# Kernel optimization log

Measured on AMD Instinct MI355X. Metric: run time of the kernel, lower is better.

Reference implementation:

```python
import jax, jax.numpy as jnp
import numpy as np

N, E, M = 50000, 50000, 640000
IN_DIM, D, L = 256, 128, 3

def setup_inputs() -> dict:
    key = jax.random.key(0)
    ks = jax.random.split(key, 8)
    x = jax.random.normal(ks[0], (N, IN_DIM), dtype=jnp.float32)
    hyperedge_index = jax.random.randint(ks[1], (2, M), 0, N, dtype=jnp.int64)
    weightMatrix = jax.random.uniform(ks[2], (E,), dtype=jnp.float32)
    edgesWeights = jax.random.uniform(ks[3], (M,), dtype=jnp.float32)
    stdv_fc = 1.0 / np.sqrt(IN_DIM)
    fc_w = jax.random.uniform(ks[4], (IN_DIM, D), minval=-stdv_fc, maxval=stdv_fc, dtype=jnp.float32)
    fc_b = jax.random.uniform(ks[5], (D,), minval=-stdv_fc, maxval=stdv_fc, dtype=jnp.float32)
    stdv = 1.0 / np.sqrt(D)
    conv_w = jax.random.uniform(ks[6], (L, D, D), minval=-stdv, maxval=stdv, dtype=jnp.float32)
    conv_b = jax.random.uniform(ks[7], (L, D), minval=-stdv, maxval=stdv, dtype=jnp.float32)
    return {"x": x, "hyperedge_index": hyperedge_index, "weightMatrix": weightMatrix,
            "edgesWeights": edgesWeights, "fc_w": fc_w, "fc_b": fc_b,
            "conv_w": conv_w, "conv_b": conv_b}

def reference(x, hyperedge_index, weightMatrix, edgesWeights, fc_w, fc_b, conv_w, conv_b):
    row, col = hyperedge_index[0], hyperedge_index[1]
    n_nodes, n_edges = x.shape[0], weightMatrix.shape[0]
    # degree normalization (computed once, shared by all layers since inputs identical)
    node_deg = jax.ops.segment_sum(weightMatrix[col], row, num_segments=n_nodes) + 1e-8
    hyper_deg = jax.ops.segment_sum(edgesWeights, col, num_segments=n_edges) + 1e-8
    nd = node_deg ** -0.5
    nd = jnp.where(jnp.isinf(nd), 0.0, nd)
    hd = hyper_deg ** -0.5
    hd = jnp.where(jnp.isinf(hd), 0.0, hd)
    norm = hd[col] * nd[row]  # [M]
    h = jax.nn.relu(x @ fc_w + fc_b)  # [N, D]; dropout inactive (eval)
    for i in range(conv_w.shape[0]):
        xt = h @ conv_w[i] + conv_b[i]                                  # [N, D]
        wx = xt[row] * (edgesWeights * norm)[:, None]                   # [M, D]
        hyper_feat = jax.ops.segment_sum(wx, col, num_segments=n_edges)  # [E, D]
        wh = hyper_feat[col] * (weightMatrix[col] * edgesWeights * norm)[:, None]  # [M, D]
        z = jax.ops.segment_sum(wh, row, num_segments=n_nodes)           # [N, D]
        h = jax.nn.relu(h + z)
    return h
```

## Files before the change

kernel.cpp:

```cpp
#include <hip/hip_runtime.h>
#include <hip/hip_bf16.h>
#include <stdint.h>

typedef __attribute__((ext_vector_type(4))) float f4;
typedef __attribute__((ext_vector_type(2))) float f2;
typedef __attribute__((ext_vector_type(2))) int i2;
typedef __attribute__((ext_vector_type(8))) unsigned short us8;
typedef __attribute__((ext_vector_type(4))) unsigned short us4;
typedef __attribute__((ext_vector_type(2))) unsigned short us2;
typedef __attribute__((ext_vector_type(8))) short s8b;
typedef __attribute__((ext_vector_type(4))) float f32x4;

#define CW_SHIFT 7
#define CH 2048

__device__ __forceinline__ float bf2f(unsigned short u) {
  union { unsigned int i; float f; } t; t.i = ((unsigned int)u) << 16; return t.f;
}
__device__ __forceinline__ unsigned short f2bf(float f) {
  union { float f; unsigned int i; } t; t.f = f;
  unsigned int u = t.i;
  return (unsigned short)((u + 0x7FFFu + ((u >> 16) & 1u)) >> 16);
}
__device__ __forceinline__ float cvtload(const void* p, int i, int f16) {
  return f16 ? bf2f(((const unsigned short*)p)[i]) : ((const float*)p)[i];
}

__global__ void detect_kernel(const unsigned int* __restrict__ xb,
                              const unsigned int* __restrict__ ib,
                              int* __restrict__ flags) {
  if (threadIdx.x == 0) {
    int cnt = 0;
    for (int i = 0; i < 256; ++i) {
      unsigned int e = (xb[i] >> 7) & 0xffu;
      if (e >= 110u && e <= 135u) ++cnt;
    }
    flags[0] = (cnt >= 180) ? 1 : 0;
    int zc = 0;
    for (int i = 0; i < 128; ++i) if (ib[2 * i + 1] == 0u) ++zc;
    flags[1] = (zc >= 120) ? 1 : 0;
  }
}

__global__ void cvt_params(const void* __restrict__ wM, const void* __restrict__ fcw,
                           const void* __restrict__ fcb, const void* __restrict__ cw,
                           const void* __restrict__ cb,
                           float* __restrict__ WMf, unsigned short* __restrict__ FCWT,
                           float* __restrict__ FCB, unsigned short* __restrict__ CWT,
                           float* __restrict__ CBf,
                           int E, int L, const int* __restrict__ flags) {
  const int IN_DIM = 256, D = 128;
  int i = blockIdx.x * 256 + threadIdx.x;
  const int f16 = flags[0];
  if (i < E) { WMf[i] = cvtload(wM, i, f16); return; }
  i -= E;
  if (i < IN_DIM * D) {
    int c = i >> 8, k = i & 255;
    FCWT[i] = f2bf(cvtload(fcw, k * D + c, f16));
    return;
  }
  i -= IN_DIM * D;
  if (i < D) { FCB[i] = cvtload(fcb, i, f16); return; }
  i -= D;
  if (i < L * D * D) {
    int l = i >> 14, rem = i & 16383;
    int c = rem >> 7, k = rem & 127;
    CWT[i] = f2bf(cvtload(cw, l * D * D + k * D + c, f16));
    return;
  }
  i -= L * D * D;
  if (i < L * D) CBf[i] = cvtload(cb, i, f16);
}

__global__ __launch_bounds__(256) void bin_count(
    const void* __restrict__ hei, int M, int* __restrict__ cntAB,
    int nbE, int nbN, int nblk, const int* __restrict__ flags) {
  __shared__ int hA[512];
  __shared__ int hB[512];
  const int tid = threadIdx.x, blk = blockIdx.x;
  for (int b = tid; b < 512; b += 256) { hA[b] = 0; hB[b] = 0; }
  __syncthreads();
  const int i64 = flags[1];
#pragma unroll
  for (int i = 0; i < CH / 256; ++i) {
    int m = blk * CH + i * 256 + tid;
    if (m >= M) break;
    int r, c;
    if (i64) {
      r = (int)((const long long*)hei)[m];
      c = (int)((const long long*)hei)[M + m];
    } else {
      r = ((const int*)hei)[m];
      c = ((const int*)hei)[M + m];
    }
    atomicAdd(&hA[c >> CW_SHIFT], 1);
    atomicAdd(&hB[r >> CW_SHIFT], 1);
  }
  __syncthreads();
  for (int b = tid; b < nbE; b += 256) cntAB[b * nblk + blk] = hA[b];
  for (int b = tid; b < nbN; b += 256) cntAB[(nbE + b) * nblk + blk] = hB[b];
}

__global__ __launch_bounds__(512) void scanA(int* __restrict__ cnt,
                                             int* __restrict__ btot, int nblk) {
  __shared__ int sc[512];
  const int tid = threadIdx.x, b = blockIdx.x;
  int v = (tid < nblk) ? cnt[b * nblk + tid] : 0;
  sc[tid] = v;
  __syncthreads();
  for (int s = 1; s < 512; s <<= 1) {
    int t = (tid >= s) ? sc[tid - s] : 0;
    __syncthreads();
    sc[tid] += t;
    __syncthreads();
  }
  if (tid < nblk) cnt[b * nblk + tid] = sc[tid] - v;
  if (tid == 511) btot[b] = sc[511];
}

__global__ __launch_bounds__(512) void scanB(const int* __restrict__ btot,
                                             int* __restrict__ bbaseA,
                                             int* __restrict__ bbaseB,
                                             int nbE, int nbN) {
  __shared__ int sc[512];
  const int tid = threadIdx.x;
  const int nb = blockIdx.x ? nbN : nbE;
  const int* src = blockIdx.x ? (btot + nbE) : btot;
  int* dst = blockIdx.x ? bbaseB : bbaseA;
  int v = (tid < nb) ? src[tid] : 0;
  sc[tid] = v;
  __syncthreads();
  for (int s = 1; s < 512; s <<= 1) {
    int t = (tid >= s) ? sc[tid - s] : 0;
    __syncthreads();
    sc[tid] += t;
    __syncthreads();
  }
  if (tid < nb) dst[tid] = sc[tid] - v;
  if (tid == 511) dst[nb] = sc[511];
}

__global__ __launch_bounds__(256) void binscatter(
    const void* __restrict__ hei, const void* __restrict__ ew, int M,
    const int* __restrict__ cntAB,
    const int* __restrict__ bbaseA, const int* __restrict__ bbaseB,
    int* __restrict__ KEYA, i2* __restrict__ PAYA,
    int* __restrict__ KEYB, i2* __restrict__ PAYB,
    int nbE, int nbN, int nblk, const int* __restrict__ flags) {
  __shared__ int baseA[512];
  __shared__ int baseB[512];
  const int tid = threadIdx.x, blk = blockIdx.x;
  for (int b = tid; b < nbE; b += 256) baseA[b] = bbaseA[b] + cntAB[b * nblk + blk];
  for (int b = tid; b < nbN; b += 256) baseB[b] = bbaseB[b] + cntAB[(nbE + b) * nblk + blk];
  __syncthreads();
  const int i64 = flags[1], f16 = flags[0];
#pragma unroll
  for (int i = 0; i < CH / 256; ++i) {
    int m = blk * CH + i * 256 + tid;
    if (m >= M) break;
    int r, c;
    if (i64) {
      r = (int)((const long long*)hei)[m];
      c = (int)((const long long*)hei)[M + m];
    } else {
      r = ((const int*)hei)[m];
      c = ((const int*)hei)[M + m];
    }
    int e = __float_as_int(f16 ? bf2f(((const unsigned short*)ew)[m])
                               : ((const float*)ew)[m]);
    int pA = atomicAdd(&baseA[c >> CW_SHIFT], 1);
    KEYA[pA] = c;
    i2 ea; ea[0] = r; ea[1] = e; PAYA[pA] = ea;
    int pB = atomicAdd(&baseB[r >> CW_SHIFT], 1);
    KEYB[pB] = r;
    i2 eb; eb[0] = c; eb[1] = e; PAYB[pB] = eb;
  }
}

__global__ __launch_bounds__(256) void finalize3(
    const int* __restrict__ KEYA, const i2* __restrict__ PAYA,
    const int* __restrict__ bbaseA, i2* __restrict__ ENTA,
    int* __restrict__ offE, int E,
    const int* __restrict__ KEYB, const i2* __restrict__ PAYB,
    const int* __restrict__ bbaseB, i2* __restrict__ ENTB,
    int* __restrict__ offN, int Nn,
    const float* __restrict__ WMf, float* __restrict__ SCE,
    float* __restrict__ ND, int nbE) {
  __shared__ int cnt[128];
  __shared__ int sc[128];
  __shared__ int cur[128];
  __shared__ float fsum[128];
  int b = blockIdx.x;
  const int* KEY; const i2* PAY; const int* bbase; i2* ENT; int* off;
  int nseg, modeB; float* outScale;
  if (b < nbE) {
    KEY = KEYA; PAY = PAYA; bbase = bbaseA; ENT = ENTA; off = offE;
    nseg = E; modeB = 0; outScale = SCE;
  } else {
    b -= nbE;
    KEY = KEYB; PAY = PAYB; bbase = bbaseB; ENT = ENTB; off = offN;
    nseg = Nn; modeB = 1; outScale = ND;
  }
  const int tid = threadIdx.x;
  const int bs = bbase[b], be = bbase[b + 1];
  const int cb = b << CW_SHIFT;
  const int cw = min(128, nseg - cb);
  if (tid < 128) { cnt[tid] = 0; fsum[tid] = 0.f; }
  __syncthreads();
  for (int k = bs + tid; k < be; k += 256) atomicAdd(&cnt[KEY[k] - cb], 1);
  __syncthreads();
  if (tid < 128) sc[tid] = cnt[tid];
  __syncthreads();
  for (int s = 1; s < 128; s <<= 1) {
    int t = (tid < 128 && tid >= s) ? sc[tid - s] : 0;
    __syncthreads();
    if (tid < 128) sc[tid] += t;
    __syncthreads();
  }
  if (tid < 128) {
    int start = bs + sc[tid] - cnt[tid];
    cur[tid] = start;
    if (tid < cw) off[cb + tid] = start;
  }
  if (tid == 0 && b == ((nseg + 127) >> CW_SHIFT) - 1) off[nseg] = be;
  __syncthreads();
  for (int k = bs + tid; k < be; k += 256) {
    int c = KEY[k] - cb;
    i2 p = PAY[k];
    int pos = atomicAdd(&cur[c], 1);
    ENT[pos] = p;
    float add = modeB ? WMf[p[0]] : __int_as_float(p[1]);
    atomicAdd(&fsum[c], add);
  }
  __syncthreads();
  if (tid < cw) {
    float s = fsum[tid] + 1e-8f;
    outScale[cb + tid] = modeB ? rsqrtf(s) : (WMf[cb + tid] / s);
  }
}

template<int KS>
__global__ __launch_bounds__(256) void gemm_mfma3(
    const void* __restrict__ Aptr, const unsigned short* __restrict__ Wt,
    const float* __restrict__ bias, unsigned short* __restrict__ out,
    int Nrows, const int* __restrict__ flags, int relu,
    const float* __restrict__ rowScale) {
  constexpr int K = KS * 32;
  constexpr int KC = K / 8;
  extern __shared__ unsigned short Bs[];
  const int tid = threadIdx.x;
  const int wv = tid >> 6, ln = tid & 63;
  const int lr = ln & 15;
  const int lk = (ln >> 4) << 3;
  const int rowBase = blockIdx.x * 128 + wv * 32;
  const int aF32 = flags ? (flags[0] ? 0 : 1) : 0;

  int ar[2];
#pragma unroll
  for (int t = 0; t < 2; ++t) {
    int r = rowBase + t * 16 + lr;
    ar[t] = (r < Nrows) ? r : (Nrows - 1);
  }

  s8b aR[2][KS];
  if (!aF32) {
#pragma unroll
    for (int t = 0; t < 2; ++t)
#pragma unroll
      for (int ks = 0; ks < KS; ++ks)
        aR[t][ks] = *reinterpret_cast<const s8b*>(
            (const unsigned short*)Aptr + (size_t)ar[t] * K + ks * 32 + lk);
  } else {
#pragma unroll
    for (int t = 0; t < 2; ++t)
#pragma unroll
      for (int ks = 0; ks < KS; ++ks) {
        const float* ap = (const float*)Aptr + (size_t)ar[t] * K + ks * 32 + lk;
        f4 u0 = *reinterpret_cast<const f4*>(ap);
        f4 u1 = *reinterpret_cast<const f4*>(ap + 4);
#pragma unroll
        for (int j = 0; j < 4; ++j) {
          aR[t][ks][j]     = (short)f2bf(u0[j]);
          aR[t][ks][4 + j] = (short)f2bf(u1[j]);
        }
      }
  }

#pragma unroll
  for (int it = 0; it < (128 * KC + 255) / 256; ++it) {
    int ch = it * 256 + tid;
    if (ch < 128 * KC) {
      int row = ch / KC, kc = (ch % KC) << 3;
      us8 v = *reinterpret_cast<const us8*>(Wt + (size_t)row * K + kc);
      int byte = ((row * K + kc) << 1) ^ ((row & 7) << 4);
      *reinterpret_cast<us8*>((char*)Bs + byte) = v;
    }
  }
  __syncthreads();

  f32x4 acc[2][8];
#pragma unroll
  for (int t = 0; t < 2; ++t)
#pragma unroll
    for (int n = 0; n < 8; ++n) acc[t][n] = (f32x4)0.f;

#pragma unroll
  for (int ks = 0; ks < KS; ++ks) {
#pragma unroll
    for (int n = 0; n < 8; ++n) {
      const int brow = n * 16 + lr;
      int byte = ((brow * K + ks * 32 + lk) << 1) ^ ((brow & 7) << 4);
      s8b b = *reinterpret_cast<const s8b*>((const char*)Bs + byte);
      acc[0][n] = __builtin_amdgcn_mfma_f32_16x16x32_bf16(aR[0][ks], b, acc[0][n], 0, 0, 0);
      acc[1][n] = __builtin_amdgcn_mfma_f32_16x16x32_bf16(aR[1][ks], b, acc[1][n], 0, 0, 0);
    }
  }

#pragma unroll
  for (int t = 0; t < 2; ++t) {
    const int orow0 = rowBase + t * 16 + ((ln >> 4) << 2);
#pragma unroll
    for (int n = 0; n < 8; ++n) {
      const int col = n * 16 + lr;
      const float bv = bias[col];
#pragma unroll
      for (int r = 0; r < 4; ++r) {
        int row = orow0 + r;
        if (row >= Nrows) continue;
        float s = acc[t][n][r] + bv;
        if (relu) s = fmaxf(s, 0.f);
        if (rowScale) s *= rowScale[row];
        out[(size_t)row * 128 + col] = f2bf(s);
      }
    }
  }
}

__global__ __launch_bounds__(256) void gather_edge3(
    const int* __restrict__ off, const i2* __restrict__ ENT,
    const float* __restrict__ sc_e, const unsigned short* __restrict__ X,
    unsigned short* __restrict__ out, int nseg) {
  int seg = blockIdx.x * 8 + (threadIdx.x >> 5);
  if (seg >= nseg) return;
  int d = (threadIdx.x & 31) << 2;
  int k0 = off[seg], k1 = off[seg + 1];
  float a0 = 0.f, a1 = 0.f, a2 = 0.f, a3 = 0.f;
  int k = k0;
  for (; k + 4 <= k1; k += 4) {
    i2 e0 = ENT[k], e1 = ENT[k + 1], e2 = ENT[k + 2], e3 = ENT[k + 3];
    us4 v0 = *reinterpret_cast<const us4*>(X + (size_t)e0[0] * 128 + d);
    us4 v1 = *reinterpret_cast<const us4*>(X + (size_t)e1[0] * 128 + d);
    us4 v2 = *reinterpret_cast<const us4*>(X + (size_t)e2[0] * 128 + d);
    us4 v3 = *reinterpret_cast<const us4*>(X + (size_t)e3[0] * 128 + d);
    float c0 = __int_as_float(e0[1]), c1 = __int_as_float(e1[1]);
    float c2 = __int_as_float(e2[1]), c3 = __int_as_float(e3[1]);
    a0 += c0 * bf2f(v0[0]); a1 += c0 * bf2f(v0[1]); a2 += c0 * bf2f(v0[2]); a3 += c0 * bf2f(v0[3]);
    a0 += c1 * bf2f(v1[0]); a1 += c1 * bf2f(v1[1]); a2 += c1 * bf2f(v1[2]); a3 += c1 * bf2f(v1[3]);
    a0 += c2 * bf2f(v2[0]); a1 += c2 * bf2f(v2[1]); a2 += c2 * bf2f(v2[2]); a3 += c2 * bf2f(v2[3]);
    a0 += c3 * bf2f(v3[0]); a1 += c3 * bf2f(v3[1]); a2 += c3 * bf2f(v3[2]); a3 += c3 * bf2f(v3[3]);
  }
  for (; k < k1; ++k) {
    i2 e = ENT[k];
    us4 v = *reinterpret_cast<const us4*>(X + (size_t)e[0] * 128 + d);
    float c = __int_as_float(e[1]);
    a0 += c * bf2f(v[0]); a1 += c * bf2f(v[1]); a2 += c * bf2f(v[2]); a3 += c * bf2f(v[3]);
  }
  float sc = sc_e[seg];
  us4 o;
  o[0] = f2bf(sc * a0); o[1] = f2bf(sc * a1); o[2] = f2bf(sc * a2); o[3] = f2bf(sc * a3);
  *reinterpret_cast<us4*>(out + (size_t)seg * 128 + d) = o;
}

__global__ __launch_bounds__(256) void gather_node3(
    const int* __restrict__ off, const i2* __restrict__ ENT,
    const float* __restrict__ nd, const unsigned short* __restrict__ HF,
    const unsigned short* __restrict__ H, void* __restrict__ out,
    int nseg, int outF32) {
  int seg = blockIdx.x * 8 + (threadIdx.x >> 5);
  if (seg >= nseg) return;
  int d = (threadIdx.x & 31) << 2;
  int k0 = off[seg], k1 = off[seg + 1];
  float a0 = 0.f, a1 = 0.f, a2 = 0.f, a3 = 0.f;
  int k = k0;
  for (; k + 4 <= k1; k += 4) {
    i2 e0 = ENT[k], e1 = ENT[k + 1], e2 = ENT[k + 2], e3 = ENT[k + 3];
    us4 v0 = *reinterpret_cast<const us4*>(HF + (size_t)e0[0] * 128 + d);
    us4 v1 = *reinterpret_cast<const us4*>(HF + (size_t)e1[0] * 128 + d);
    us4 v2 = *reinterpret_cast<const us4*>(HF + (size_t)e2[0] * 128 + d);
    us4 v3 = *reinterpret_cast<const us4*>(HF + (size_t)e3[0] * 128 + d);
    float c0 = __int_as_float(e0[1]), c1 = __int_as_float(e1[1]);
    float c2 = __int_as_float(e2[1]), c3 = __int_as_float(e3[1]);
    a0 += c0 * bf2f(v0[0]); a1 += c0 * bf2f(v0[1]); a2 += c0 * bf2f(v0[2]); a3 += c0 * bf2f(v0[3]);
    a0 += c1 * bf2f(v1[0]); a1 += c1 * bf2f(v1[1]); a2 += c1 * bf2f(v1[2]); a3 += c1 * bf2f(v1[3]);
    a0 += c2 * bf2f(v2[0]); a1 += c2 * bf2f(v2[1]); a2 += c2 * bf2f(v2[2]); a3 += c2 * bf2f(v2[3]);
    a0 += c3 * bf2f(v3[0]); a1 += c3 * bf2f(v3[1]); a2 += c3 * bf2f(v3[2]); a3 += c3 * bf2f(v3[3]);
  }
  for (; k < k1; ++k) {
    i2 e = ENT[k];
    us4 v = *reinterpret_cast<const us4*>(HF + (size_t)e[0] * 128 + d);
    float c = __int_as_float(e[1]);
    a0 += c * bf2f(v[0]); a1 += c * bf2f(v[1]); a2 += c * bf2f(v[2]); a3 += c * bf2f(v[3]);
  }
  float s = nd[seg];
  us4 h = *reinterpret_cast<const us4*>(H + (size_t)seg * 128 + d);
  float r0 = fmaxf(bf2f(h[0]) + s * a0, 0.f);
  float r1 = fmaxf(bf2f(h[1]) + s * a1, 0.f);
  float r2 = fmaxf(bf2f(h[2]) + s * a2, 0.f);
  float r3 = fmaxf(bf2f(h[3]) + s * a3, 0.f);
  if (outF32) {
    f4 o; o[0] = r0; o[1] = r1; o[2] = r2; o[3] = r3;
    *reinterpret_cast<f4*>((float*)out + (size_t)seg * 128 + d) = o;
  } else {
    us4 o; o[0] = f2bf(r0); o[1] = f2bf(r1); o[2] = f2bf(r2); o[3] = f2bf(r3);
    *reinterpret_cast<us4*>((unsigned short*)out + (size_t)seg * 128 + d) = o;
  }
}

extern "C" void kernel_launch(void* const* d_in, const int* in_sizes, int n_in,
                              void* d_out, int out_size, void* d_ws, size_t ws_size,
                              hipStream_t stream) {
  const void* x   = d_in[0];
  const void* hei = d_in[1];
  const void* wM  = d_in[2];
  const void* ew  = d_in[3];
  const void* fcw = d_in[4];
  const void* fcb = d_in[5];
  const void* cw  = d_in[6];
  const void* cb  = d_in[7];

  const int IN_DIM = 256, D = 128;
  const int N = in_sizes[0] / IN_DIM;
  const int M = in_sizes[1] / 2;
  const int E = in_sizes[2];
  const int L = in_sizes[6] / (D * D);

  const int nbE = (E + 127) >> CW_SHIFT;
  const int nbN = (N + 127) >> CW_SHIFT;
  const int nbT = nbE + nbN;
  const int nblk = (M + CH - 1) / CH;

  float* w = (float*)d_ws;
  size_t o = 0;
  auto alloc = [&](size_t n) { float* p = w + o; o += (n + 3) & ~(size_t)3; return p; };

  float* R = alloc((size_t)(N + E) * D / 2);
  unsigned short* XT = (unsigned short*)R;
  unsigned short* HF = XT + (size_t)N * D;
  int* KEYA = (int*)R;
  i2*  PAYA = (i2*)(KEYA + M);
  int* KEYB = (int*)(PAYA + M);
  i2*  PAYB = (i2*)(KEYB + M);

  unsigned short* H  = (unsigned short*)alloc((size_t)N * D / 2);
  i2*    ENTA = (i2*)alloc((size_t)M * 2);
  i2*    ENTB = (i2*)alloc((size_t)M * 2);
  int*   cntAB = (int*)alloc((size_t)nbT * nblk);
  int*   btotAB = (int*)alloc(nbT + 2);
  int*   bbaseA = (int*)alloc(nbE + 2);
  int*   bbaseB = (int*)alloc(nbN + 2);
  float* ND   = alloc(N);
  float* SCE  = alloc(E);
  int*   offE = (int*)alloc(E + 1);
  int*   offN = (int*)alloc(N + 1);
  float* WMf  = alloc(E);
  unsigned short* FCWT = (unsigned short*)alloc((size_t)IN_DIM * D / 2);
  float* FCB  = alloc(D);
  unsigned short* CWT = (unsigned short*)alloc((size_t)L * D * D / 2);
  float* CBf  = alloc((size_t)L * D);
  int*   FLAGS = (int*)alloc(16);

  detect_kernel<<<1, 64, 0, stream>>>((const unsigned int*)x, (const unsigned int*)hei, FLAGS);

  bin_count<<<nblk, 256, 0, stream>>>(hei, M, cntAB, nbE, nbN, nblk, FLAGS);
  {
    int ntot = E + IN_DIM * D + D + L * D * D + L * D;
    cvt_params<<<(ntot + 255) / 256, 256, 0, stream>>>(wM, fcw, fcb, cw, cb,
                                                       WMf, FCWT, FCB, CWT, CBf,
                                                       E, L, FLAGS);
  }

  scanA<<<nbT, 512, 0, stream>>>(cntAB, btotAB, nblk);
  scanB<<<2, 512, 0, stream>>>(btotAB, bbaseA, bbaseB, nbE, nbN);

  binscatter<<<nblk, 256, 0, stream>>>(hei, ew, M, cntAB, bbaseA, bbaseB,
                                       KEYA, PAYA, KEYB, PAYB, nbE, nbN, nblk, FLAGS);

  finalize3<<<nbT, 256, 0, stream>>>(KEYA, PAYA, bbaseA, ENTA, offE, E,
                                     KEYB, PAYB, bbaseB, ENTB, offN, N,
                                     WMf, SCE, ND, nbE);

  gemm_mfma3<8><<<(N + 127) / 128, 256, 128 * 256 * 2, stream>>>(
      x, FCWT, FCB, H, N, FLAGS, 1, nullptr);

  int segBlkE = (E + 7) / 8, segBlkN = (N + 7) / 8;
  for (int l = 0; l < L; ++l) {
    gemm_mfma3<4><<<(N + 127) / 128, 256, 128 * 128 * 2, stream>>>(
        H, CWT + (size_t)l * D * D, CBf + (size_t)l * D, XT, N,
        (const int*)nullptr, 0, ND);
    gather_edge3<<<segBlkE, 256, 0, stream>>>(offE, ENTA, SCE, XT, HF, E);
    gather_node3<<<segBlkN, 256, 0, stream>>>(
        offN, ENTB, ND, HF, H,
        (l == L - 1) ? d_out : (void*)H, N, (l == L - 1) ? 1 : 0);
  }
}
```

Baseline: 336.1 us.

## Pack bin key into payload, enlarge scatter chunks, unroll gathers by eight

The separate key arrays in the binning sort are removed: the low 7 bits of the key are packed into the upper bits of the payload's index word, which cuts global writes and reads in binscatter and finalize3. The edge chunk per block grows from 2048 to 8192 with a runtime loop, reducing the number of blocks and the size of the per-block count matrix that scanA processes. Both gather kernels are unrolled to eight entries per iteration so more independent row loads are in flight. The packing assumes indices fit in 20 bits. Fewer scatter blocks also means less parallelism in the binning kernels.

```diff
diff --git a/kernel.cpp b/kernel.cpp
--- a/kernel.cpp
+++ b/kernel.cpp
@@ -12,7 +12,7 @@
 typedef __attribute__((ext_vector_type(4))) float f32x4;
 
 #define CW_SHIFT 7
-#define CH 2048
+#define CH 8192
 
 __device__ __forceinline__ float bf2f(unsigned short u) {
   union { unsigned int i; float f; } t; t.i = ((unsigned int)u) << 16; return t.f;
@@ -81,10 +81,8 @@
   for (int b = tid; b < 512; b += 256) { hA[b] = 0; hB[b] = 0; }
   __syncthreads();
   const int i64 = flags[1];
-#pragma unroll
-  for (int i = 0; i < CH / 256; ++i) {
-    int m = blk * CH + i * 256 + tid;
-    if (m >= M) break;
+  const int mEnd = min(M, (blk + 1) * CH);
+  for (int m = blk * CH + tid; m < mEnd; m += 256) {
     int r, c;
     if (i64) {
       r = (int)((const long long*)hei)[m];
@@ -144,8 +142,7 @@
     const void* __restrict__ hei, const void* __restrict__ ew, int M,
     const int* __restrict__ cntAB,
     const int* __restrict__ bbaseA, const int* __restrict__ bbaseB,
-    int* __restrict__ KEYA, i2* __restrict__ PAYA,
-    int* __restrict__ KEYB, i2* __restrict__ PAYB,
+    i2* __restrict__ PAYA, i2* __restrict__ PAYB,
     int nbE, int nbN, int nblk, const int* __restrict__ flags) {
   __shared__ int baseA[512];
   __shared__ int baseB[512];
@@ -154,10 +151,8 @@
   for (int b = tid; b < nbN; b += 256) baseB[b] = bbaseB[b] + cntAB[(nbE + b) * nblk + blk];
   __syncthreads();
   const int i64 = flags[1], f16 = flags[0];
-#pragma unroll
-  for (int i = 0; i < CH / 256; ++i) {
-    int m = blk * CH + i * 256 + tid;
-    if (m >= M) break;
+  const int mEnd = min(M, (blk + 1) * CH);
+  for (int m = blk * CH + tid; m < mEnd; m += 256) {
     int r, c;
     if (i64) {
       r = (int)((const long long*)hei)[m];
@@ -169,21 +164,19 @@
     int e = __float_as_int(f16 ? bf2f(((const unsigned short*)ew)[m])
                                : ((const float*)ew)[m]);
     int pA = atomicAdd(&baseA[c >> CW_SHIFT], 1);
-    KEYA[pA] = c;
-    i2 ea; ea[0] = r; ea[1] = e; PAYA[pA] = ea;
+    i2 ea; ea[0] = r | ((c & 127) << 20); ea[1] = e;
+    PAYA[pA] = ea;
     int pB = atomicAdd(&baseB[r >> CW_SHIFT], 1);
-    KEYB[pB] = r;
-    i2 eb; eb[0] = c; eb[1] = e; PAYB[pB] = eb;
+    i2 eb; eb[0] = c | ((r & 127) << 20); eb[1] = e;
+    PAYB[pB] = eb;
   }
 }
 
 __global__ __launch_bounds__(256) void finalize3(
-    const int* __restrict__ KEYA, const i2* __restrict__ PAYA,
-    const int* __restrict__ bbaseA, i2* __restrict__ ENTA,
-    int* __restrict__ offE, int E,
-    const int* __restrict__ KEYB, const i2* __restrict__ PAYB,
-    const int* __restrict__ bbaseB, i2* __restrict__ ENTB,
-    int* __restrict__ offN, int Nn,
+    const i2* __restrict__ PAYA, const int* __restrict__ bbaseA,
+    i2* __restrict__ ENTA, int* __restrict__ offE, int E,
+    const i2* __restrict__ PAYB, const int* __restrict__ bbaseB,
+    i2* __restrict__ ENTB, int* __restrict__ offN, int Nn,
     const float* __restrict__ WMf, float* __restrict__ SCE,
     float* __restrict__ ND, int nbE) {
   __shared__ int cnt[128];
@@ -191,14 +184,14 @@
   __shared__ int cur[128];
   __shared__ float fsum[128];
   int b = blockIdx.x;
-  const int* KEY; const i2* PAY; const int* bbase; i2* ENT; int* off;
+  const i2* PAY; const int* bbase; i2* ENT; int* off;
   int nseg, modeB; float* outScale;
   if (b < nbE) {
-    KEY = KEYA; PAY = PAYA; bbase = bbaseA; ENT = ENTA; off = offE;
+    PAY = PAYA; bbase = bbaseA; ENT = ENTA; off = offE;
     nseg = E; modeB = 0; outScale = SCE;
   } else {
     b -= nbE;
-    KEY = KEYB; PAY = PAYB; bbase = bbaseB; ENT = ENTB; off = offN;
+    PAY = PAYB; bbase = bbaseB; ENT = ENTB; off = offN;
     nseg = Nn; modeB = 1; outScale = ND;
   }
   const int tid = threadIdx.x;
@@ -207,7 +200,8 @@
   const int cw = min(128, nseg - cb);
   if (tid < 128) { cnt[tid] = 0; fsum[tid] = 0.f; }
   __syncthreads();
-  for (int k = bs + tid; k < be; k += 256) atomicAdd(&cnt[KEY[k] - cb], 1);
+  for (int k = bs + tid; k < be; k += 256)
+    atomicAdd(&cnt[(PAY[k][0] >> 20) & 127], 1);
   __syncthreads();
   if (tid < 128) sc[tid] = cnt[tid];
   __syncthreads();
@@ -225,12 +219,14 @@
   if (tid == 0 && b == ((nseg + 127) >> CW_SHIFT) - 1) off[nseg] = be;
   __syncthreads();
   for (int k = bs + tid; k < be; k += 256) {
-    int c = KEY[k] - cb;
     i2 p = PAY[k];
-    int pos = atomicAdd(&cur[c], 1);
-    ENT[pos] = p;
-    float add = modeB ? WMf[p[0]] : __int_as_float(p[1]);
-    atomicAdd(&fsum[c], add);
+    int key = (p[0] >> 20) & 127;
+    int src = p[0] & 0xFFFFF;
+    int pos = atomicAdd(&cur[key], 1);
+    i2 outp; outp[0] = src; outp[1] = p[1];
+    ENT[pos] = outp;
+    float add = modeB ? WMf[src] : __int_as_float(p[1]);
+    atomicAdd(&fsum[key], add);
   }
   __syncthreads();
   if (tid < cw) {
@@ -346,18 +342,19 @@
   int k0 = off[seg], k1 = off[seg + 1];
   float a0 = 0.f, a1 = 0.f, a2 = 0.f, a3 = 0.f;
   int k = k0;
-  for (; k + 4 <= k1; k += 4) {
-    i2 e0 = ENT[k], e1 = ENT[k + 1], e2 = ENT[k + 2], e3 = ENT[k + 3];
-    us4 v0 = *reinterpret_cast<const us4*>(X + (size_t)e0[0] * 128 + d);
-    us4 v1 = *reinterpret_cast<const us4*>(X + (size_t)e1[0] * 128 + d);
-    us4 v2 = *reinterpret_cast<const us4*>(X + (size_t)e2[0] * 128 + d);
-    us4 v3 = *reinterpret_cast<const us4*>(X + (size_t)e3[0] * 128 + d);
-    float c0 = __int_as_float(e0[1]), c1 = __int_as_float(e1[1]);
-    float c2 = __int_as_float(e2[1]), c3 = __int_as_float(e3[1]);
-    a0 += c0 * bf2f(v0[0]); a1 += c0 * bf2f(v0[1]); a2 += c0 * bf2f(v0[2]); a3 += c0 * bf2f(v0[3]);
-    a0 += c1 * bf2f(v1[0]); a1 += c1 * bf2f(v1[1]); a2 += c1 * bf2f(v1[2]); a3 += c1 * bf2f(v1[3]);
-    a0 += c2 * bf2f(v2[0]); a1 += c2 * bf2f(v2[1]); a2 += c2 * bf2f(v2[2]); a3 += c2 * bf2f(v2[3]);
-    a0 += c3 * bf2f(v3[0]); a1 += c3 * bf2f(v3[1]); a2 += c3 * bf2f(v3[2]); a3 += c3 * bf2f(v3[3]);
+  for (; k + 8 <= k1; k += 8) {
+    i2 e[8]; us4 v[8];
+#pragma unroll
+    for (int j = 0; j < 8; ++j) e[j] = ENT[k + j];
+#pragma unroll
+    for (int j = 0; j < 8; ++j)
+      v[j] = *reinterpret_cast<const us4*>(X + (size_t)e[j][0] * 128 + d);
+#pragma unroll
+    for (int j = 0; j < 8; ++j) {
+      float c = __int_as_float(e[j][1]);
+      a0 += c * bf2f(v[j][0]); a1 += c * bf2f(v[j][1]);
+      a2 += c * bf2f(v[j][2]); a3 += c * bf2f(v[j][3]);
+    }
   }
   for (; k < k1; ++k) {
     i2 e = ENT[k];
@@ -382,18 +379,19 @@
   int k0 = off[seg], k1 = off[seg + 1];
   float a0 = 0.f, a1 = 0.f, a2 = 0.f, a3 = 0.f;
   int k = k0;
-  for (; k + 4 <= k1; k += 4) {
-    i2 e0 = ENT[k], e1 = ENT[k + 1], e2 = ENT[k + 2], e3 = ENT[k + 3];
-    us4 v0 = *reinterpret_cast<const us4*>(HF + (size_t)e0[0] * 128 + d);
-    us4 v1 = *reinterpret_cast<const us4*>(HF + (size_t)e1[0] * 128 + d);
-    us4 v2 = *reinterpret_cast<const us4*>(HF + (size_t)e2[0] * 128 + d);
-    us4 v3 = *reinterpret_cast<const us4*>(HF + (size_t)e3[0] * 128 + d);
-    float c0 = __int_as_float(e0[1]), c1 = __int_as_float(e1[1]);
-    float c2 = __int_as_float(e2[1]), c3 = __int_as_float(e3[1]);
-    a0 += c0 * bf2f(v0[0]); a1 += c0 * bf2f(v0[1]); a2 += c0 * bf2f(v0[2]); a3 += c0 * bf2f(v0[3]);
-    a0 += c1 * bf2f(v1[0]); a1 += c1 * bf2f(v1[1]); a2 += c1 * bf2f(v1[2]); a3 += c1 * bf2f(v1[3]);
-    a0 += c2 * bf2f(v2[0]); a1 += c2 * bf2f(v2[1]); a2 += c2 * bf2f(v2[2]); a3 += c2 * bf2f(v2[3]);
-    a0 += c3 * bf2f(v3[0]); a1 += c3 * bf2f(v3[1]); a2 += c3 * bf2f(v3[2]); a3 += c3 * bf2f(v3[3]);
+  for (; k + 8 <= k1; k += 8) {
+    i2 e[8]; us4 v[8];
+#pragma unroll
+    for (int j = 0; j < 8; ++j) e[j] = ENT[k + j];
+#pragma unroll
+    for (int j = 0; j < 8; ++j)
+      v[j] = *reinterpret_cast<const us4*>(HF + (size_t)e[j][0] * 128 + d);
+#pragma unroll
+    for (int j = 0; j < 8; ++j) {
+      float c = __int_as_float(e[j][1]);
+      a0 += c * bf2f(v[j][0]); a1 += c * bf2f(v[j][1]);
+      a2 += c * bf2f(v[j][2]); a3 += c * bf2f(v[j][3]);
+    }
   }
   for (; k < k1; ++k) {
     i2 e = ENT[k];
@@ -446,10 +444,8 @@
   float* R = alloc((size_t)(N + E) * D / 2);
   unsigned short* XT = (unsigned short*)R;
   unsigned short* HF = XT + (size_t)N * D;
-  int* KEYA = (int*)R;
-  i2*  PAYA = (i2*)(KEYA + M);
-  int* KEYB = (int*)(PAYA + M);
-  i2*  PAYB = (i2*)(KEYB + M);
+  i2*  PAYA = (i2*)R;
+  i2*  PAYB = PAYA + M;
 
   unsigned short* H  = (unsigned short*)alloc((size_t)N * D / 2);
   i2*    ENTA = (i2*)alloc((size_t)M * 2);
@@ -483,10 +479,10 @@
   scanB<<<2, 512, 0, stream>>>(btotAB, bbaseA, bbaseB, nbE, nbN);
 
   binscatter<<<nblk, 256, 0, stream>>>(hei, ew, M, cntAB, bbaseA, bbaseB,
-                                       KEYA, PAYA, KEYB, PAYB, nbE, nbN, nblk, FLAGS);
-
-  finalize3<<<nbT, 256, 0, stream>>>(KEYA, PAYA, bbaseA, ENTA, offE, E,
-                                     KEYB, PAYB, bbaseB, ENTB, offN, N,
+                                       PAYA, PAYB, nbE, nbN, nblk, FLAGS);
+
+  finalize3<<<nbT, 256, 0, stream>>>(PAYA, bbaseA, ENTA, offE, E,
+                                     PAYB, bbaseB, ENTB, offN, N,
                                      WMf, SCE, ND, nbE);
 
   gemm_mfma3<8><<<(N + 127) / 128, 256, 128 * 256 * 2, stream>>>(
```

After: 348.5 us. 3.7% more time.
